# Optimization experiments

Hardware: AMD Instinct MI355X
Metric: run time of the kernel (lower is better)

Reference implementation:

```python
import jax, jax.numpy as jnp
import numpy as np

B, H, W, C = 32, 56, 56, 192
WS, SS, NH = 7, 3, 6
HD = C // NH
SCALE = HD ** -0.5
N = WS * WS
NW = (H // WS) * (W // WS)
EPS = 1e-5


def _rel_pos_index():
    coords = np.stack(np.meshgrid(np.arange(WS), np.arange(WS), indexing='ij'))  # (2,WS,WS)
    cf = coords.reshape(2, -1)
    rel = cf[:, :, None] - cf[:, None, :]  # (2,N,N)
    rel = rel.transpose(1, 2, 0)
    rel[:, :, 0] += WS - 1
    rel[:, :, 1] += WS - 1
    rel[:, :, 0] *= 2 * WS - 1
    return rel.sum(-1)  # (N,N) int


def _attn_mask():
    img = np.zeros((H, W))
    cnt = 0
    for hs in (slice(0, -WS), slice(-WS, -SS), slice(-SS, None)):
        for ws in (slice(0, -WS), slice(-WS, -SS), slice(-SS, None)):
            img[hs, ws] = cnt
            cnt += 1
    win = img.reshape(H // WS, WS, W // WS, WS).transpose(0, 2, 1, 3).reshape(NW, N)
    diff = win[:, None, :] - win[:, :, None]
    return np.where(diff != 0, -100.0, 0.0).astype(np.float32)  # (NW,N,N)


REL_IDX = jnp.asarray(_rel_pos_index())
ATTN_MASK = jnp.asarray(_attn_mask())


def _ln(x, g, b):
    mu = x.mean(-1, keepdims=True)
    var = ((x - mu) ** 2).mean(-1, keepdims=True)
    return (x - mu) * jax.lax.rsqrt(var + EPS) * g + b


def setup_inputs() -> dict:
    key = jax.random.key(0)
    ks = jax.random.split(key, 8)
    d = {
        'x': jax.random.normal(ks[0], (B, H * W, C), jnp.float32),
        'norm1_g': jnp.ones((C,), jnp.float32),
        'norm1_b': jnp.zeros((C,), jnp.float32),
        'qkv_w': jax.random.normal(ks[1], (C, 3 * C), jnp.float32) * 0.02,
        'qkv_b': jnp.zeros((3 * C,), jnp.float32),
        'rpb_table': jax.random.normal(ks[2], ((2 * WS - 1) ** 2, NH), jnp.float32) * 0.02,
        'proj_w': jax.random.normal(ks[3], (C, C), jnp.float32) * 0.02,
        'proj_b': jnp.zeros((C,), jnp.float32),
        'norm2_g': jnp.ones((C,), jnp.float32),
        'norm2_b': jnp.zeros((C,), jnp.float32),
        'fc1_w': jax.random.normal(ks[4], (C, 4 * C), jnp.float32) * 0.02,
        'fc1_b': jnp.zeros((4 * C,), jnp.float32),
        'fc2_w': jax.random.normal(ks[5], (4 * C, C), jnp.float32) * 0.02,
        'fc2_b': jnp.zeros((C,), jnp.float32),
    }
    return d


def reference(x, norm1_g, norm1_b, qkv_w, qkv_b, rpb_table, proj_w, proj_b,
              norm2_g, norm2_b, fc1_w, fc1_b, fc2_w, fc2_b):
    shortcut = x
    h = _ln(x, norm1_g, norm1_b).reshape(B, H, W, C)
    # cyclic shift
    h = jnp.roll(h, (-SS, -SS), axis=(1, 2))
    # window partition -> (B*NW, N, C)
    hw = h.reshape(B, H // WS, WS, W // WS, WS, C).transpose(0, 1, 3, 2, 4, 5)
    hw = hw.reshape(B * NW, N, C)
    # qkv
    qkv = (hw @ qkv_w + qkv_b).reshape(B * NW, N, 3, NH, HD).transpose(2, 0, 3, 1, 4)
    q, k, v = qkv[0], qkv[1], qkv[2]  # (B_, NH, N, HD)
    attn = jnp.einsum('whnd,whmd->whnm', q * SCALE, k)
    bias = rpb_table[REL_IDX.reshape(-1)].reshape(N, N, NH).transpose(2, 0, 1)
    attn = attn + bias[None]
    # shift mask
    attn = attn.reshape(B, NW, NH, N, N) + ATTN_MASK[None, :, None]
    attn = jax.nn.softmax(attn.reshape(B * NW, NH, N, N), axis=-1)
    out = jnp.einsum('whnm,whmd->whnd', attn, v).transpose(0, 2, 1, 3).reshape(B * NW, N, C)
    out = out @ proj_w + proj_b
    # window reverse + unshift
    out = out.reshape(B, H // WS, W // WS, WS, WS, C).transpose(0, 1, 3, 2, 4, 5).reshape(B, H, W, C)
    out = jnp.roll(out, (SS, SS), axis=(1, 2)).reshape(B, H * W, C)
    x = shortcut + out
    # MLP
    m = _ln(x, norm2_g, norm2_b)
    m = jax.nn.gelu(m @ fc1_w + fc1_b, approximate=False) @ fc2_w + fc2_b
    return x + m
```

## Files before the change

### kernel.cpp

```cpp
#include <hip/hip_runtime.h>
#include <hip/hip_bf16.h>
#include <math.h>

#define MTOK 100352
#define SCALE_ 0.17677669529663687f

typedef short bf16x8 __attribute__((ext_vector_type(8)));
typedef float f32x4 __attribute__((ext_vector_type(4)));

__device__ __forceinline__ float b2f(unsigned short u) {
    return __uint_as_float(((unsigned int)u) << 16);
}
__device__ __forceinline__ unsigned short f2b(float f) {
    unsigned int u = __float_as_uint(f);
    unsigned int r = (u + 0x7FFFu + ((u >> 16) & 1u)) >> 16;
    return (unsigned short)r;
}
__device__ __forceinline__ void gload_lds16(const unsigned short* g, unsigned short* l) {
    __builtin_amdgcn_global_load_lds(
        (const __attribute__((address_space(1))) void*)g,
        (__attribute__((address_space(3))) void*)l, 16, 0, 0);
}

__global__ __launch_bounds__(256) void wconv_k(
    const float* __restrict__ w, unsigned short* __restrict__ wt, int K, int N)
{
    const int i = blockIdx.x * 256 + threadIdx.x;
    if (i >= N * K) return;
    const int n = i / K, k = i - n * K;
    wt[i] = f2b(w[(size_t)k * N + n]);
}

__global__ __launch_bounds__(256) void ln1_window_k(
    const float* __restrict__ x, const float* __restrict__ g,
    const float* __restrict__ bt, unsigned short* __restrict__ out)
{
    const int wid = (blockIdx.x * 256 + threadIdx.x) >> 6;
    if (wid >= MTOK) return;
    const int lane = threadIdx.x & 63;
    const int widx = wid / 49, n = wid - widx * 49;
    const int b = widx >> 6, win = widx & 63;
    const int wh = win >> 3, ww = win & 7;
    const int r = n / 7, cc = n - r * 7;
    int hh = wh * 7 + r + 3;  if (hh >= 56) hh -= 56;
    int wc = ww * 7 + cc + 3; if (wc >= 56) wc -= 56;
    const size_t src = ((size_t)b * 3136 + hh * 56 + wc) * 192;
    const float v0 = x[src + lane], v1 = x[src + lane + 64], v2 = x[src + lane + 128];
    float s1 = v0 + v1 + v2;
    float s2 = v0 * v0 + v1 * v1 + v2 * v2;
    #pragma unroll
    for (int off = 32; off; off >>= 1) {
        s1 += __shfl_xor(s1, off, 64);
        s2 += __shfl_xor(s2, off, 64);
    }
    const float mu = s1 * (1.f / 192.f);
    const float var = s2 * (1.f / 192.f) - mu * mu;
    const float rs = rsqrtf(var + 1e-5f);
    const size_t dst = (size_t)wid * 192;
    out[dst + lane]       = f2b((v0 - mu) * rs * g[lane]       + bt[lane]);
    out[dst + lane + 64]  = f2b((v1 - mu) * rs * g[lane + 64]  + bt[lane + 64]);
    out[dst + lane + 128] = f2b((v2 - mu) * rs * g[lane + 128] + bt[lane + 128]);
}

__global__ __launch_bounds__(256) void ln2_k(
    const float* __restrict__ x, const float* __restrict__ g,
    const float* __restrict__ bt, unsigned short* __restrict__ out)
{
    const int t = (blockIdx.x * 256 + threadIdx.x) >> 6;
    if (t >= MTOK) return;
    const int lane = threadIdx.x & 63;
    const size_t src = (size_t)t * 192;
    const float v0 = x[src + lane], v1 = x[src + lane + 64], v2 = x[src + lane + 128];
    float s1 = v0 + v1 + v2;
    float s2 = v0 * v0 + v1 * v1 + v2 * v2;
    #pragma unroll
    for (int off = 32; off; off >>= 1) {
        s1 += __shfl_xor(s1, off, 64);
        s2 += __shfl_xor(s2, off, 64);
    }
    const float mu = s1 * (1.f / 192.f);
    const float var = s2 * (1.f / 192.f) - mu * mu;
    const float rs = rsqrtf(var + 1e-5f);
    out[src + lane]       = f2b((v0 - mu) * rs * g[lane]       + bt[lane]);
    out[src + lane + 64]  = f2b((v1 - mu) * rs * g[lane + 64]  + bt[lane + 64]);
    out[src + lane + 128] = f2b((v2 - mu) * rs * g[lane + 128] + bt[lane + 128]);
}

enum { EPI_STORE_BF16 = 0, EPI_PROJ = 1, EPI_GELU = 2, EPI_RES = 3 };

template <int EPI>
__global__ __launch_bounds__(256) void mgemm_k(
    const unsigned short* __restrict__ A, const unsigned short* __restrict__ BT,
    const float* __restrict__ bias, unsigned short* __restrict__ outb,
    float* __restrict__ outf, const float* __restrict__ xres,
    int N, int K, int gx)
{
    __shared__ __align__(16) unsigned short As[2][256 * 32];
    __shared__ __align__(16) unsigned short Bs[2][64 * 32];

    const int nwg = gridDim.x;
    int lin = blockIdx.x;
    lin = (lin & 7) * (nwg >> 3) + (lin >> 3);
    const int bn = lin % gx, bm = lin / gx;
    const int row0 = bm * 256, col0 = bn * 64;

    const int tid = threadIdx.x;
    const int w = tid >> 6, lane = tid & 63;
    const int l16 = lane & 15, l4 = lane >> 4;

    const unsigned short* Ab = A + (size_t)row0 * K;
    const unsigned short* Bb = BT + (size_t)col0 * K;
    const int sr = lane >> 2;
    const int sq = ((lane & 3) ^ ((lane >> 3) & 3)) * 8;

    #pragma unroll
    for (int i = 0; i < 4; i++) {
        const int ch = w * 4 + i;
        gload_lds16(Ab + (size_t)(ch * 16 + sr) * K + sq, &As[0][ch * 512 + lane * 8]);
    }
    gload_lds16(Bb + (size_t)(w * 16 + sr) * K + sq, &Bs[0][w * 512 + lane * 8]);
    __syncthreads();

    f32x4 acc[4][4];
    #pragma unroll
    for (int m = 0; m < 4; m++)
        #pragma unroll
        for (int n = 0; n < 4; n++) acc[m][n] = (f32x4){0.f, 0.f, 0.f, 0.f};

    const int rdc = (l4 ^ ((l16 >> 1) & 3)) * 8;
    const int nt = K >> 5;
    for (int t = 0; t < nt; ++t) {
        const int cur = t & 1;
        if (t + 1 < nt) {
            const int k0 = (t + 1) << 5;
            #pragma unroll
            for (int i = 0; i < 4; i++) {
                const int ch = w * 4 + i;
                gload_lds16(Ab + (size_t)(ch * 16 + sr) * K + k0 + sq,
                            &As[cur ^ 1][ch * 512 + lane * 8]);
            }
            gload_lds16(Bb + (size_t)(w * 16 + sr) * K + k0 + sq,
                        &Bs[cur ^ 1][w * 512 + lane * 8]);
        }
        bf16x8 af[4], bf[4];
        #pragma unroll
        for (int m = 0; m < 4; m++)
            af[m] = *reinterpret_cast<const bf16x8*>(
                &As[cur][(w * 64 + m * 16 + l16) * 32 + rdc]);
        #pragma unroll
        for (int n = 0; n < 4; n++)
            bf[n] = *reinterpret_cast<const bf16x8*>(
                &Bs[cur][(n * 16 + l16) * 32 + rdc]);
        #pragma unroll
        for (int m = 0; m < 4; m++)
            #pragma unroll
            for (int n = 0; n < 4; n++)
                acc[m][n] = __builtin_amdgcn_mfma_f32_16x16x32_bf16(
                    af[m], bf[n], acc[m][n], 0, 0, 0);
        __syncthreads();
    }

    float bv[4];
    #pragma unroll
    for (int n = 0; n < 4; n++) bv[n] = bias[col0 + n * 16 + l16];

    #pragma unroll
    for (int m = 0; m < 4; m++) {
        #pragma unroll
        for (int j = 0; j < 4; j++) {
            const int row = row0 + w * 64 + m * 16 + l4 * 4 + j;
            if constexpr (EPI == EPI_PROJ) {
                const int widx = row / 49, n49 = row - widx * 49;
                const int b = widx >> 6, win = widx & 63;
                const int wh = win >> 3, ww = win & 7;
                const int r = n49 / 7, cc = n49 - r * 7;
                int hh = wh * 7 + r + 3;  if (hh >= 56) hh -= 56;
                int wcc = ww * 7 + cc + 3; if (wcc >= 56) wcc -= 56;
                const size_t tok = ((size_t)b * 3136 + hh * 56 + wcc) * 192;
                #pragma unroll
                for (int n = 0; n < 4; n++) {
                    const int col = col0 + n * 16 + l16;
                    outf[tok + col] = xres[tok + col] + acc[m][n][j] + bv[n];
                }
            } else if constexpr (EPI == EPI_STORE_BF16) {
                #pragma unroll
                for (int n = 0; n < 4; n++) {
                    const int col = col0 + n * 16 + l16;
                    outb[(size_t)row * N + col] = f2b(acc[m][n][j] + bv[n]);
                }
            } else if constexpr (EPI == EPI_GELU) {
                #pragma unroll
                for (int n = 0; n < 4; n++) {
                    const int col = col0 + n * 16 + l16;
                    float v = acc[m][n][j] + bv[n];
                    v = 0.5f * v * (1.f + erff(v * 0.70710678118654752f));
                    outb[(size_t)row * N + col] = f2b(v);
                }
            } else {
                #pragma unroll
                for (int n = 0; n < 4; n++) {
                    const int col = col0 + n * 16 + l16;
                    outf[(size_t)row * N + col] += acc[m][n][j] + bv[n];
                }
            }
        }
    }
}

__global__ __launch_bounds__(64) void attn_mfma_k(
    const unsigned short* __restrict__ qkv, const float* __restrict__ rpb,
    unsigned short* __restrict__ out)
{
    const int blk = blockIdx.x;
    const int widx = blk / 6, head = blk - widx * 6;
    const int win = widx & 63;
    const int wh = win >> 3, ww = win & 7;

    __shared__ __align__(16) unsigned short vt[32 * 72];
    __shared__ __align__(16) unsigned short pl[64 * 72];
    __shared__ float bias_s[256];

    const int lane = threadIdx.x;
    const int l16 = lane & 15, l4 = lane >> 4;
    const size_t base = (size_t)widx * 49 * 576 + (size_t)head * 32;

    for (int i = lane; i < 169; i += 64) bias_s[i] = rpb[i * 6 + head];

    #pragma unroll
    for (int it = 0; it < 4; ++it) {
        const int c = lane + it * 64;
        const int m = c >> 2, d8 = (c & 3) * 8;
        bf16x8 v8 = {};
        if (m < 49)
            v8 = *reinterpret_cast<const bf16x8*>(qkv + base + (size_t)m * 576 + 384 + d8);
        #pragma unroll
        for (int r = 0; r < 8; ++r) vt[(d8 + r) * 72 + m] = (unsigned short)v8[r];
    }

    bf16x8 kf[4], qf[4];
    #pragma unroll
    for (int f = 0; f < 4; ++f) {
        const int rrow = f * 16 + l16;
        bf16x8 kz = {}, qz = {};
        if (rrow < 49) {
            kz = *reinterpret_cast<const bf16x8*>(qkv + base + (size_t)rrow * 576 + 192 + l4 * 8);
            qz = *reinterpret_cast<const bf16x8*>(qkv + base + (size_t)rrow * 576 + l4 * 8);
        }
        kf[f] = kz; qf[f] = qz;
    }

    f32x4 acc[4][4];
    #pragma unroll
    for (int mf = 0; mf < 4; ++mf)
        #pragma unroll
        for (int nf = 0; nf < 4; ++nf) {
            f32x4 z = (f32x4){0.f, 0.f, 0.f, 0.f};
            acc[mf][nf] = __builtin_amdgcn_mfma_f32_16x16x32_bf16(kf[mf], qf[nf], z, 0, 0, 0);
        }

    __syncthreads();

    int gn[4], labn[4]; bool nok[4];
    #pragma unroll
    for (int nf = 0; nf < 4; ++nf) {
        const int n = nf * 16 + l16;
        const int rn = (n * 9363) >> 16, cn = n - rn * 7;
        gn[nf] = n + 6 * rn;
        labn[nf] = (wh == 7 ? (rn < 4 ? 1 : 2) : 0) * 3 + (ww == 7 ? (cn < 4 ? 1 : 2) : 0);
        nok[nf] = (n < 49);
    }

    #pragma unroll
    for (int mf = 0; mf < 4; ++mf) {
        #pragma unroll
        for (int j = 0; j < 4; ++j) {
            const int m = mf * 16 + l4 * 4 + j;
            const int rm = (m * 9363) >> 16, cm = m - rm * 7;
            const int gm = m + 6 * rm;
            const int labm = (wh == 7 ? (rm < 4 ? 1 : 2) : 0) * 3 + (ww == 7 ? (cm < 4 ? 1 : 2) : 0);
            const bool mok = (m < 49);
            #pragma unroll
            for (int nf = 0; nf < 4; ++nf) {
                float s = -1e30f;
                if (mok && nok[nf]) {
                    s = acc[mf][nf][j] * SCALE_ + bias_s[gn[nf] - gm + 84];
                    if (labn[nf] != labm) s -= 100.f;
                }
                acc[mf][nf][j] = s;
            }
        }
    }

    #pragma unroll
    for (int nf = 0; nf < 4; ++nf) {
        float mx = -1e30f;
        #pragma unroll
        for (int mf = 0; mf < 4; ++mf)
            #pragma unroll
            for (int j = 0; j < 4; ++j) mx = fmaxf(mx, acc[mf][nf][j]);
        mx = fmaxf(mx, __shfl_xor(mx, 16, 64));
        mx = fmaxf(mx, __shfl_xor(mx, 32, 64));
        float sum = 0.f;
        #pragma unroll
        for (int mf = 0; mf < 4; ++mf)
            #pragma unroll
            for (int j = 0; j < 4; ++j) {
                const float e = __expf(acc[mf][nf][j] - mx);
                acc[mf][nf][j] = e;
                sum += e;
            }
        sum += __shfl_xor(sum, 16, 64);
        sum += __shfl_xor(sum, 32, 64);
        const float inv = 1.f / sum;
        const int n = nf * 16 + l16;
        #pragma unroll
        for (int mf = 0; mf < 4; ++mf)
            #pragma unroll
            for (int jp = 0; jp < 2; ++jp) {
                const int m = mf * 16 + l4 * 4 + jp * 2;
                const unsigned int pk =
                    (unsigned int)f2b(acc[mf][nf][jp * 2] * inv) |
                    ((unsigned int)f2b(acc[mf][nf][jp * 2 + 1] * inv) << 16);
                *reinterpret_cast<unsigned int*>(&pl[n * 72 + m]) = pk;
            }
    }
    __syncthreads();

    f32x4 oacc[4][2];
    #pragma unroll
    for (int nf = 0; nf < 4; ++nf)
        #pragma unroll
        for (int df = 0; df < 2; ++df) oacc[nf][df] = (f32x4){0.f, 0.f, 0.f, 0.f};
    #pragma unroll
    for (int ks = 0; ks < 2; ++ks) {
        bf16x8 vf[2];
        #pragma unroll
        for (int df = 0; df < 2; ++df)
            vf[df] = *reinterpret_cast<const bf16x8*>(&vt[(df * 16 + l16) * 72 + ks * 32 + l4 * 8]);
        #pragma unroll
        for (int nf = 0; nf < 4; ++nf) {
            const bf16x8 pf = *reinterpret_cast<const bf16x8*>(&pl[(nf * 16 + l16) * 72 + ks * 32 + l4 * 8]);
            #pragma unroll
            for (int df = 0; df < 2; ++df)
                oacc[nf][df] = __builtin_amdgcn_mfma_f32_16x16x32_bf16(pf, vf[df], oacc[nf][df], 0, 0, 0);
        }
    }

    #pragma unroll
    for (int nf = 0; nf < 4; ++nf)
        #pragma unroll
        for (int j = 0; j < 4; ++j) {
            const int n = nf * 16 + l4 * 4 + j;
            if (n < 49) {
                const size_t o = ((size_t)widx * 49 + n) * 192 + (size_t)head * 32;
                out[o + l16]      = f2b(oacc[nf][0][j]);
                out[o + 16 + l16] = f2b(oacc[nf][1][j]);
            }
        }
}

extern "C" void kernel_launch(void* const* d_in, const int* in_sizes, int n_in,
                              void* d_out, int out_size, void* d_ws, size_t ws_size,
                              hipStream_t stream)
{
    const float* x      = (const float*)d_in[0];
    const float* n1g    = (const float*)d_in[1];
    const float* n1b    = (const float*)d_in[2];
    const float* qkv_w  = (const float*)d_in[3];
    const float* qkv_b  = (const float*)d_in[4];
    const float* rpb    = (const float*)d_in[5];
    const float* proj_w = (const float*)d_in[6];
    const float* proj_b = (const float*)d_in[7];
    const float* n2g    = (const float*)d_in[8];
    const float* n2b    = (const float*)d_in[9];
    const float* fc1_w  = (const float*)d_in[10];
    const float* fc1_b  = (const float*)d_in[11];
    const float* fc2_w  = (const float*)d_in[12];
    const float* fc2_b  = (const float*)d_in[13];
    float* out = (float*)d_out;

    const int M = MTOK;
    unsigned short* big   = (unsigned short*)d_ws;
    unsigned short* winx  = big + (size_t)M * 768;
    unsigned short* qkvT  = winx + (size_t)M * 192;
    unsigned short* projT = qkvT + 576 * 192;
    unsigned short* fc1T  = projT + 192 * 192;
    unsigned short* fc2T  = fc1T + 768 * 192;

    wconv_k<<<(576 * 192 + 255) / 256, 256, 0, stream>>>(qkv_w, qkvT, 192, 576);
    wconv_k<<<(192 * 192 + 255) / 256, 256, 0, stream>>>(proj_w, projT, 192, 192);
    wconv_k<<<(768 * 192 + 255) / 256, 256, 0, stream>>>(fc1_w, fc1T, 192, 768);
    wconv_k<<<(192 * 768 + 255) / 256, 256, 0, stream>>>(fc2_w, fc2T, 768, 192);

    ln1_window_k<<<M / 4, 256, 0, stream>>>(x, n1g, n1b, winx);
    mgemm_k<EPI_STORE_BF16><<<9 * (M / 256), 256, 0, stream>>>(
        winx, qkvT, qkv_b, big, nullptr, nullptr, 576, 192, 9);
    attn_mfma_k<<<2048 * 6, 64, 0, stream>>>(big, rpb, winx);
    mgemm_k<EPI_PROJ><<<3 * (M / 256), 256, 0, stream>>>(
        winx, projT, proj_b, nullptr, out, x, 192, 192, 3);
    ln2_k<<<M / 4, 256, 0, stream>>>(out, n2g, n2b, winx);
    mgemm_k<EPI_GELU><<<12 * (M / 256), 256, 0, stream>>>(
        winx, fc1T, fc1_b, big, nullptr, nullptr, 768, 192, 12);
    mgemm_k<EPI_RES><<<3 * (M / 256), 256, 0, stream>>>(
        big, fc2T, fc2_b, nullptr, out, nullptr, 192, 768, 3);
}
```

Measured before the change: 393.6 us.

## Load GEMM A operand directly to registers, stage B in large LDS chunks, tanh GELU

```diff
diff --git a/kernel.cpp b/kernel.cpp
--- a/kernel.cpp
+++ b/kernel.cpp
@@ -88,15 +88,17 @@
 
 enum { EPI_STORE_BF16 = 0, EPI_PROJ = 1, EPI_GELU = 2, EPI_RES = 3 };
 
-template <int EPI>
+template <int EPI, int K>
 __global__ __launch_bounds__(256) void mgemm_k(
     const unsigned short* __restrict__ A, const unsigned short* __restrict__ BT,
     const float* __restrict__ bias, unsigned short* __restrict__ outb,
     float* __restrict__ outf, const float* __restrict__ xres,
-    int N, int K, int gx)
-{
-    __shared__ __align__(16) unsigned short As[2][256 * 32];
-    __shared__ __align__(16) unsigned short Bs[2][64 * 32];
+    int N, int gx)
+{
+    constexpr int KC = (K < 256) ? K : 256;
+    constexpr int NCH = KC / 32;
+    constexpr int NKC = K / KC;
+    __shared__ __align__(16) unsigned short Bs[64 * KC];
 
     const int nwg = gridDim.x;
     int lin = blockIdx.x;
@@ -108,18 +110,12 @@
     const int w = tid >> 6, lane = tid & 63;
     const int l16 = lane & 15, l4 = lane >> 4;
 
-    const unsigned short* Ab = A + (size_t)row0 * K;
     const unsigned short* Bb = BT + (size_t)col0 * K;
     const int sr = lane >> 2;
     const int sq = ((lane & 3) ^ ((lane >> 3) & 3)) * 8;
-
-    #pragma unroll
-    for (int i = 0; i < 4; i++) {
-        const int ch = w * 4 + i;
-        gload_lds16(Ab + (size_t)(ch * 16 + sr) * K + sq, &As[0][ch * 512 + lane * 8]);
-    }
-    gload_lds16(Bb + (size_t)(w * 16 + sr) * K + sq, &Bs[0][w * 512 + lane * 8]);
-    __syncthreads();
+    const int rdc = (l4 ^ ((l16 >> 1) & 3)) * 8;
+
+    const unsigned short* Aw = A + (size_t)(row0 + w * 64 + l16) * K + l4 * 8;
 
     f32x4 acc[4][4];
     #pragma unroll
@@ -127,37 +123,34 @@
         #pragma unroll
         for (int n = 0; n < 4; n++) acc[m][n] = (f32x4){0.f, 0.f, 0.f, 0.f};
 
-    const int rdc = (l4 ^ ((l16 >> 1) & 3)) * 8;
-    const int nt = K >> 5;
-    for (int t = 0; t < nt; ++t) {
-        const int cur = t & 1;
-        if (t + 1 < nt) {
-            const int k0 = (t + 1) << 5;
-            #pragma unroll
-            for (int i = 0; i < 4; i++) {
-                const int ch = w * 4 + i;
-                gload_lds16(Ab + (size_t)(ch * 16 + sr) * K + k0 + sq,
-                            &As[cur ^ 1][ch * 512 + lane * 8]);
-            }
-            gload_lds16(Bb + (size_t)(w * 16 + sr) * K + k0 + sq,
-                        &Bs[cur ^ 1][w * 512 + lane * 8]);
-        }
-        bf16x8 af[4], bf[4];
-        #pragma unroll
-        for (int m = 0; m < 4; m++)
-            af[m] = *reinterpret_cast<const bf16x8*>(
-                &As[cur][(w * 64 + m * 16 + l16) * 32 + rdc]);
-        #pragma unroll
-        for (int n = 0; n < 4; n++)
-            bf[n] = *reinterpret_cast<const bf16x8*>(
-                &Bs[cur][(n * 16 + l16) * 32 + rdc]);
-        #pragma unroll
-        for (int m = 0; m < 4; m++)
+    for (int kc = 0; kc < NKC; ++kc) {
+        const int kbase = kc * KC;
+        #pragma unroll
+        for (int p = w; p < NCH * 4; p += 4) {
+            const int ck = p >> 2, rg = p & 3;
+            gload_lds16(Bb + (size_t)(rg * 16 + sr) * K + kbase + ck * 32 + sq,
+                        &Bs[ck * 2048 + rg * 512 + lane * 8]);
+        }
+        __syncthreads();
+        #pragma unroll
+        for (int ks = 0; ks < NCH; ++ks) {
+            const int k = kbase + ks * 32;
+            bf16x8 af[4], bf[4];
+            #pragma unroll
+            for (int m = 0; m < 4; m++)
+                af[m] = *reinterpret_cast<const bf16x8*>(Aw + (size_t)(m * 16) * K + k);
             #pragma unroll
             for (int n = 0; n < 4; n++)
-                acc[m][n] = __builtin_amdgcn_mfma_f32_16x16x32_bf16(
-                    af[m], bf[n], acc[m][n], 0, 0, 0);
-        __syncthreads();
+                bf[n] = *reinterpret_cast<const bf16x8*>(
+                    &Bs[ks * 2048 + (n * 16 + l16) * 32 + rdc]);
+            #pragma unroll
+            for (int m = 0; m < 4; m++)
+                #pragma unroll
+                for (int n = 0; n < 4; n++)
+                    acc[m][n] = __builtin_amdgcn_mfma_f32_16x16x32_bf16(
+                        af[m], bf[n], acc[m][n], 0, 0, 0);
+        }
+        if (kc + 1 < NKC) __syncthreads();
     }
 
     float bv[4];
@@ -193,7 +186,10 @@
                 for (int n = 0; n < 4; n++) {
                     const int col = col0 + n * 16 + l16;
                     float v = acc[m][n][j] + bv[n];
-                    v = 0.5f * v * (1.f + erff(v * 0.70710678118654752f));
+                    const float y = 0.7978845608028654f * (v + 0.044715f * v * v * v);
+                    const float e2 = __expf(2.f * y);
+                    const float th = 1.f - 2.f / (e2 + 1.f);
+                    v = 0.5f * v * (1.f + th);
                     outb[(size_t)row * N + col] = f2b(v);
                 }
             } else {
@@ -393,14 +389,14 @@
     wconv_k<<<(192 * 768 + 255) / 256, 256, 0, stream>>>(fc2_w, fc2T, 768, 192);
 
     ln1_window_k<<<M / 4, 256, 0, stream>>>(x, n1g, n1b, winx);
-    mgemm_k<EPI_STORE_BF16><<<9 * (M / 256), 256, 0, stream>>>(
-        winx, qkvT, qkv_b, big, nullptr, nullptr, 576, 192, 9);
+    mgemm_k<EPI_STORE_BF16, 192><<<9 * (M / 256), 256, 0, stream>>>(
+        winx, qkvT, qkv_b, big, nullptr, nullptr, 576, 9);
     attn_mfma_k<<<2048 * 6, 64, 0, stream>>>(big, rpb, winx);
-    mgemm_k<EPI_PROJ><<<3 * (M / 256), 256, 0, stream>>>(
-        winx, projT, proj_b, nullptr, out, x, 192, 192, 3);
+    mgemm_k<EPI_PROJ, 192><<<3 * (M / 256), 256, 0, stream>>>(
+        winx, projT, proj_b, nullptr, out, x, 192, 3);
     ln2_k<<<M / 4, 256, 0, stream>>>(out, n2g, n2b, winx);
-    mgemm_k<EPI_GELU><<<12 * (M / 256), 256, 0, stream>>>(
-        winx, fc1T, fc1_b, big, nullptr, nullptr, 768, 192, 12);
-    mgemm_k<EPI_RES><<<3 * (M / 256), 256, 0, stream>>>(
-        big, fc2T, fc2_b, nullptr, out, nullptr, 192, 768, 3);
-}
+    mgemm_k<EPI_GELU, 192><<<12 * (M / 256), 256, 0, stream>>>(
+        winx, fc1T, fc1_b, big, nullptr, nullptr, 768, 12);
+    mgemm_k<EPI_RES, 768><<<3 * (M / 256), 256, 0, stream>>>(
+        big, fc2T, fc2_b, nullptr, out, nullptr, 192, 3);
+}
```

New measurement: 440.8 us. 1.12x slower.
